# Optimization experiments

Hardware: AMD Instinct MI355X
Metric: run time of the kernel (lower is better)

## Reference

```python
import jax, jax.numpy as jnp
import numpy as np

C = 8            # number of categories (len(cat_id_radius_order_map_list))
S = 4            # segments per category
RADIUS_START = 1.0
RADIUS_DIFF = 1.0
MARGIN = -2.0    # cosine_emb_loss_margin; clamp(dot - MARGIN, 0) is identity since dot >= -1
RW = 0.5         # radius_loss_weight
SW = 0.5         # similarity_loss_weight
EPS = 1e-6


def setup_inputs() -> dict:
    key = jax.random.key(0)
    B, D, H, W = 4, 32, 512, 512
    outputs = jax.random.normal(key, (B, D, H, W), dtype=jnp.float32)
    # structured panoptic masks: C*S segments, contiguous in row-major flat order
    P = (H * W) // (C * S)                 # pixels per segment
    seg = (jnp.arange(H * W) // P).reshape(H, W).astype(jnp.int32)   # channel 0: segment id
    cat = (seg // S).astype(jnp.int32)                                # channel 1: category id
    inst = jnp.ones((H, W), jnp.int32)                                # channel 2: instance-discr flag (all True)
    masks = jnp.broadcast_to(jnp.stack([seg, cat, inst], axis=0)[None], (B, 3, H, W)).astype(jnp.int32)
    return {"outputs": outputs, "masks": masks, "annotations_data": 0}


def reference(outputs, masks, annotations_data):
    B, D, H, W = outputs.shape
    HW = H * W
    Sn = C * S
    P = HW // Sn
    emb = outputs.reshape(B, D, HW).transpose(0, 2, 1)          # [B, HW, D]
    seg_flat = masks[:, 0].reshape(B, HW)
    cat_flat = masks[:, 1].reshape(B, HW)
    radii = RADIUS_START + RADIUS_DIFF * jnp.arange(C, dtype=jnp.float32)

    # ---- radius loss: per-category MSE(||emb||_2, radius_cat), skipping the first unique cat (0)
    norms = jnp.linalg.norm(emb, axis=-1)                       # [B, HW]
    err = (norms - radii[cat_flat]) ** 2
    cat_all = cat_flat.reshape(-1)
    sums = jax.ops.segment_sum(err.reshape(-1), cat_all, num_segments=C)
    cnts = jax.ops.segment_sum(jnp.ones((B * HW,), jnp.float32), cat_all, num_segments=C)
    per_cat_mse = sums / cnts
    radius_loss = jnp.mean(per_cat_mse[1:])                     # unique_cat_ids[1:] -> cats 1..C-1

    # ---- gather pixels per segment; stable sort by segment id == boolean-mask gather order
    order = jnp.argsort(seg_flat, axis=1, stable=True)          # [B, HW]
    emb_sorted = jnp.take_along_axis(emb, order[..., None], axis=1)
    segs = emb_sorted.reshape(B, C, S, P, D)                    # segments grouped by category
    v = segs / (jnp.linalg.norm(segs, axis=-1, keepdims=True) + EPS)  # per-pixel L2-normalize

    count = P * (P + 1) / 2.0                                   # upper triangle incl diagonal

    # positives: mean over triu(incl diag) of (1 - v_i . v_j)
    #   sum_{triu} gram = (||sum_p v_p||^2 + sum_p ||v_p||^2) / 2
    T = jnp.sum(jnp.sum(v, axis=3) ** 2, axis=-1)               # [B, C, S]
    Dg = jnp.sum(v ** 2, axis=(3, 4))                           # [B, C, S]
    pos_mean = 1.0 - (T + Dg) / (2.0 * count)
    pos_total = jnp.sum(pos_mean)

    # negatives (same cat, segment pairs i<j): mean over triu(incl diag) of clamp(gram - MARGIN, 0)
    # clamp is inactive for MARGIN=-2; triu row-sum via reverse inclusive cumsum over pixels of j
    R = jnp.cumsum(v[:, :, :, ::-1, :], axis=3)[:, :, :, ::-1, :]     # [B, C, S, P, D]
    pair = jnp.einsum('bcipd,bcjpd->bcij', v, R)                # triu-sum of gram(curr=i, neg=j)
    iu, ju = jnp.triu_indices(S, k=1)
    neg_mean = pair[:, :, iu, ju] / count - MARGIN              # [B, C, S*(S-1)/2]
    neg_total = jnp.sum(neg_mean)

    sim_counter = B * C * (S + S * (S - 1) // 2)
    similarity_loss = (pos_total + neg_total) / sim_counter
    return RW * radius_loss + SW * similarity_loss
```

## Files before the change

### kernel.cpp

```cpp
#include <hip/hip_runtime.h>
#include <hip/hip_bf16.h>
#include <cstdint>

#define C_ 8
#define Bn 4
#define Dn 32
#define HWn 262144
#define Pn 8192
#define CH 256
#define NCH 32
#define NBLK (Bn*C_*NCH)
#define COUNTF 33558528.0f
#define CNT_PER_CAT 131072.0f

#define WS_SUM 0
#define WS_PART (NBLK*4*32)
#define WS_BC (WS_PART + NBLK*16)

__device__ __forceinline__ float wred(float x){
  #pragma unroll
  for (int off = 32; off; off >>= 1) x += __shfl_xor(x, off, 64);
  return x;
}

__device__ __forceinline__ unsigned int bfr(float x){
  __hip_bfloat16 h = __float2bfloat16(x);
  return (unsigned int)*reinterpret_cast<unsigned short*>(&h);
}

#define UNPK_LO(w) __uint_as_float((w) << 16)
#define UNPK_HI(w) __uint_as_float((w) & 0xffff0000u)

#define STEP(a0,a1,a2,a3) { \
  r0 += a0; r1 += a1; r2 += a2; r3 += a3; \
  p01 = fmaf(r0,a1,p01); p02 = fmaf(r0,a2,p02); p03 = fmaf(r0,a3,p03); \
  p12 = fmaf(r1,a2,p12); p13 = fmaf(r1,a3,p13); p23 = fmaf(r2,a3,p23); }

#define STEPW(w0,w1,w2,w3) { \
  STEP(UNPK_LO(w0), UNPK_LO(w1), UNPK_LO(w2), UNPK_LO(w3)); \
  STEP(UNPK_HI(w0), UNPK_HI(w1), UNPK_HI(w2), UNPK_HI(w3)); }

__global__ __launch_bounds__(256) void kA(const float* __restrict__ src, float* __restrict__ ws){
  __shared__ __align__(16) __hip_bfloat16 vbuf[4][32][264];
  __shared__ float lsum[4][32][8];
  __shared__ float redbuf[4][8];
  const int tid = threadIdx.x;
  const int blk = blockIdx.x;
  const int b = blk >> 8;
  const int c = (blk >> 5) & 7;
  const int k = blk & 31;
  const int j = tid >> 6;
  const int l = tid & 63;
  const float radius = 1.0f + (float)c;

  float errAcc = 0.0f, dgAcc = 0.0f;
  {
    const float* gp = src + (size_t)b*Dn*HWn + (size_t)(c*4+j)*Pn + (size_t)k*CH + l*4;
    float4 x[32];
    #pragma unroll
    for (int d = 0; d < 32; ++d) x[d] = *reinterpret_cast<const float4*>(gp + (size_t)d*HWn);
    float n0=0.f, n1=0.f, n2=0.f, n3=0.f;
    #pragma unroll
    for (int d = 0; d < 32; ++d){
      n0 = fmaf(x[d].x, x[d].x, n0); n1 = fmaf(x[d].y, x[d].y, n1);
      n2 = fmaf(x[d].z, x[d].z, n2); n3 = fmaf(x[d].w, x[d].w, n3);
    }
    float m0 = sqrtf(n0), m1 = sqrtf(n1), m2 = sqrtf(n2), m3 = sqrtf(n3);
    float i0 = 1.0f/(m0+1e-6f), i1 = 1.0f/(m1+1e-6f);
    float i2 = 1.0f/(m2+1e-6f), i3 = 1.0f/(m3+1e-6f);
    float e0 = m0-radius, e1 = m1-radius, e2 = m2-radius, e3 = m3-radius;
    errAcc = fmaf(e0,e0, fmaf(e1,e1, fmaf(e2,e2, e3*e3)));
    dgAcc  = fmaf(n0*i0,i0, fmaf(n1*i1,i1, fmaf(n2*i2,i2, (n3*i3)*i3)));
    #pragma unroll
    for (int d = 0; d < 32; ++d){
      unsigned int u0 = bfr(x[d].x*i0) | (bfr(x[d].y*i1) << 16);
      unsigned int u1 = bfr(x[d].z*i2) | (bfr(x[d].w*i3) << 16);
      *reinterpret_cast<uint2*>(&vbuf[j][d][l*4]) = make_uint2(u0, u1);
    }
  }
  __syncthreads();

  const int d = tid & 31;
  const int s = tid >> 5;
  float r0=0,r1=0,r2=0,r3=0;
  float p01=0,p02=0,p03=0,p12=0,p13=0,p23=0;
  {
    const uint4* s0p = (const uint4*)&vbuf[0][d][32*s];
    const uint4* s1p = (const uint4*)&vbuf[1][d][32*s];
    const uint4* s2p = (const uint4*)&vbuf[2][d][32*s];
    const uint4* s3p = (const uint4*)&vbuf[3][d][32*s];
    #pragma unroll
    for (int g = 0; g < 4; ++g){
      uint4 A = s0p[g], B = s1p[g], Cq = s2p[g], Dq = s3p[g];
      STEPW(A.x, B.x, Cq.x, Dq.x);
      STEPW(A.y, B.y, Cq.y, Dq.y);
      STEPW(A.z, B.z, Cq.z, Dq.z);
      STEPW(A.w, B.w, Cq.w, Dq.w);
    }
  }
  lsum[0][d][s] = r0; lsum[1][d][s] = r1; lsum[2][d][s] = r2; lsum[3][d][s] = r3;

  p01 = wred(p01); p02 = wred(p02); p03 = wred(p03);
  p12 = wred(p12); p13 = wred(p13); p23 = wred(p23);
  float dg = wred(dgAcc);
  float er = wred(errAcc);
  if ((tid & 63) == 0){
    const int w = tid >> 6;
    redbuf[w][0]=p01; redbuf[w][1]=p02; redbuf[w][2]=p03;
    redbuf[w][3]=p12; redbuf[w][4]=p13; redbuf[w][5]=p23;
    redbuf[w][6]=dg;  redbuf[w][7]=er;
  }
  __syncthreads();
  if (tid >= 64) return;

  float c0=0,c1=0,c2=0,c3=0;
  float x01=0,x02=0,x03=0,x12=0,x13=0,x23=0;
  {
    const int dd = tid & 31;
    #pragma unroll
    for (int ss = 0; ss < 8; ++ss){
      float a0=lsum[0][dd][ss], a1=lsum[1][dd][ss], a2=lsum[2][dd][ss], a3=lsum[3][dd][ss];
      x01=fmaf(c0,a1,x01); x02=fmaf(c0,a2,x02); x03=fmaf(c0,a3,x03);
      x12=fmaf(c1,a2,x12); x13=fmaf(c1,a3,x13); x23=fmaf(c2,a3,x23);
      c0+=a0; c1+=a1; c2+=a2; c3+=a3;
    }
    if (tid < 32){
      float* sp = ws + WS_SUM + (size_t)blk*128 + dd;
      sp[0]=c0; sp[32]=c1; sp[64]=c2; sp[96]=c3;
    }
  }
  x01 = 0.5f*wred(x01); x02 = 0.5f*wred(x02); x03 = 0.5f*wred(x03);
  x12 = 0.5f*wred(x12); x13 = 0.5f*wred(x13); x23 = 0.5f*wred(x23);
  if (tid == 0){
    float* pp = ws + WS_PART + (size_t)blk*16;
    pp[0] = redbuf[0][0]+redbuf[1][0]+redbuf[2][0]+redbuf[3][0] + x01;
    pp[1] = redbuf[0][1]+redbuf[1][1]+redbuf[2][1]+redbuf[3][1] + x02;
    pp[2] = redbuf[0][2]+redbuf[1][2]+redbuf[2][2]+redbuf[3][2] + x03;
    pp[3] = redbuf[0][3]+redbuf[1][3]+redbuf[2][3]+redbuf[3][3] + x12;
    pp[4] = redbuf[0][4]+redbuf[1][4]+redbuf[2][4]+redbuf[3][4] + x13;
    pp[5] = redbuf[0][5]+redbuf[1][5]+redbuf[2][5]+redbuf[3][5] + x23;
    pp[6] = redbuf[0][6]; pp[7] = redbuf[1][6];
    pp[8] = redbuf[2][6]; pp[9] = redbuf[3][6];
    pp[10] = redbuf[0][7]+redbuf[1][7]+redbuf[2][7]+redbuf[3][7];
  }
}

__global__ __launch_bounds__(64) void kB(float* __restrict__ ws){
  const int bc = blockIdx.x;
  const int lane = threadIdx.x;
  const int d = lane & 31;
  float c0=0,c1=0,c2=0,c3=0;
  float x01=0,x02=0,x03=0,x12=0,x13=0,x23=0;
  #pragma unroll 4
  for (int k = 0; k < 32; ++k){
    const float* sp = ws + WS_SUM + (size_t)(bc*32+k)*128 + d;
    float a0=sp[0], a1=sp[32], a2=sp[64], a3=sp[96];
    x01=fmaf(c0,a1,x01); x02=fmaf(c0,a2,x02); x03=fmaf(c0,a3,x03);
    x12=fmaf(c1,a2,x12); x13=fmaf(c1,a3,x13); x23=fmaf(c2,a3,x23);
    c0+=a0; c1+=a1; c2+=a2; c3+=a3;
  }
  float T0 = 0.5f*wred(c0*c0), T1 = 0.5f*wred(c1*c1);
  float T2 = 0.5f*wred(c2*c2), T3 = 0.5f*wred(c3*c3);
  x01=0.5f*wred(x01); x02=0.5f*wred(x02); x03=0.5f*wred(x03);
  x12=0.5f*wred(x12); x13=0.5f*wred(x13); x23=0.5f*wred(x23);

  const float* pp = ws + WS_PART + (size_t)(bc*32 + d)*16;
  float q0 = 0.5f*wred(pp[0]), q1 = 0.5f*wred(pp[1]), q2 = 0.5f*wred(pp[2]);
  float q3 = 0.5f*wred(pp[3]), q4 = 0.5f*wred(pp[4]), q5 = 0.5f*wred(pp[5]);
  float q6 = 0.5f*wred(pp[6]), q7 = 0.5f*wred(pp[7]), q8 = 0.5f*wred(pp[8]);
  float q9 = 0.5f*wred(pp[9]), q10 = 0.5f*wred(pp[10]);

  if (lane == 0){
    const float inv2c = 1.0f/(2.0f*COUNTF);
    const float invc  = 1.0f/COUNTF;
    float pos = (1.0f-(T0+q6)*inv2c) + (1.0f-(T1+q7)*inv2c)
              + (1.0f-(T2+q8)*inv2c) + (1.0f-(T3+q9)*inv2c);
    float neg = ((x01+q0)*invc + 2.0f) + ((x02+q1)*invc + 2.0f) + ((x03+q2)*invc + 2.0f)
              + ((x12+q3)*invc + 2.0f) + ((x13+q4)*invc + 2.0f) + ((x23+q5)*invc + 2.0f);
    float* o = ws + WS_BC + bc*3;
    o[0]=q10; o[1]=pos; o[2]=neg;
  }
}

__global__ __launch_bounds__(64) void kC(const float* __restrict__ ws, float* __restrict__ out){
  const int lane = threadIdx.x;
  float er = 0.f, pn = 0.f;
  if (lane < 32){
    const float* o = ws + WS_BC + lane*3;
    er = o[0]; pn = o[1] + o[2];
  }
  float sv = pn;
  #pragma unroll
  for (int off = 32; off; off >>= 1) sv += __shfl_xor(sv, off, 64);
  er += __shfl_xor(er, 8, 64);
  er += __shfl_xor(er, 16, 64);
  float r = (lane >= 1 && lane < 8) ? (er / CNT_PER_CAT) : 0.0f;
  r += __shfl_xor(r, 1, 64);
  r += __shfl_xor(r, 2, 64);
  r += __shfl_xor(r, 4, 64);
  if (lane == 0){
    float radius_loss = r / 7.0f;
    float sim = sv / 320.0f;
    out[0] = 0.5f*radius_loss + 0.5f*sim;
  }
}

extern "C" void kernel_launch(void* const* d_in, const int* in_sizes, int n_in,
                              void* d_out, int out_size, void* d_ws, size_t ws_size,
                              hipStream_t stream){
  const float* outputs = (const float*)d_in[0];
  float* ws  = (float*)d_ws;
  float* out = (float*)d_out;
  kA<<<NBLK, 256, 0, stream>>>(outputs, ws);
  kB<<<32, 64, 0, stream>>>(ws);
  kC<<<1, 64, 0, stream>>>(ws, out);
}
```

Before: 199.4 us.

## Split fused kernel into normalize-to-bf16 global stage and pair-product stage

```diff
diff --git a/kernel.cpp b/kernel.cpp
--- a/kernel.cpp
+++ b/kernel.cpp
@@ -1,5 +1,4 @@
 #include <hip/hip_runtime.h>
-#include <hip/hip_bf16.h>
 #include <cstdint>
 
 #define C_ 8
@@ -7,25 +6,19 @@
 #define Dn 32
 #define HWn 262144
 #define Pn 8192
-#define CH 256
-#define NCH 32
-#define NBLK (Bn*C_*NCH)
 #define COUNTF 33558528.0f
 #define CNT_PER_CAT 131072.0f
 
-#define WS_SUM 0
-#define WS_PART (NBLK*4*32)
-#define WS_BC (WS_PART + NBLK*16)
+#define WS_SUM  16777216
+#define WS_PART (WS_SUM + 131072)
+#define WS_DG   (WS_PART + 8192)
+#define WS_ERR  (WS_DG + 4096)
+#define WS_BC   (WS_ERR + 4096)
 
 __device__ __forceinline__ float wred(float x){
   #pragma unroll
   for (int off = 32; off; off >>= 1) x += __shfl_xor(x, off, 64);
   return x;
-}
-
-__device__ __forceinline__ unsigned int bfr(float x){
-  __hip_bfloat16 h = __float2bfloat16(x);
-  return (unsigned int)*reinterpret_cast<unsigned short*>(&h);
 }
 
 #define UNPK_LO(w) __uint_as_float((w) << 16)
@@ -40,55 +33,70 @@
   STEP(UNPK_LO(w0), UNPK_LO(w1), UNPK_LO(w2), UNPK_LO(w3)); \
   STEP(UNPK_HI(w0), UNPK_HI(w1), UNPK_HI(w2), UNPK_HI(w3)); }
 
-__global__ __launch_bounds__(256) void kA(const float* __restrict__ src, float* __restrict__ ws){
-  __shared__ __align__(16) __hip_bfloat16 vbuf[4][32][264];
-  __shared__ float lsum[4][32][8];
-  __shared__ float redbuf[4][8];
+__global__ __launch_bounds__(256) void kS(const float* __restrict__ src, float* __restrict__ ws){
   const int tid = threadIdx.x;
   const int blk = blockIdx.x;
-  const int b = blk >> 8;
-  const int c = (blk >> 5) & 7;
-  const int k = blk & 31;
-  const int j = tid >> 6;
-  const int l = tid & 63;
+  const int r = blk & 7;
+  const int j = (blk >> 3) & 3;
+  const int bc = blk >> 5;
+  const int b = bc >> 3, c = bc & 7;
+  const int w = tid >> 6;
+  const int k = (r << 2) | w;
+  const int pos = (r << 10) + tid * 4;
   const float radius = 1.0f + (float)c;
 
-  float errAcc = 0.0f, dgAcc = 0.0f;
-  {
-    const float* gp = src + (size_t)b*Dn*HWn + (size_t)(c*4+j)*Pn + (size_t)k*CH + l*4;
-    float4 x[32];
-    #pragma unroll
-    for (int d = 0; d < 32; ++d) x[d] = *reinterpret_cast<const float4*>(gp + (size_t)d*HWn);
-    float n0=0.f, n1=0.f, n2=0.f, n3=0.f;
-    #pragma unroll
-    for (int d = 0; d < 32; ++d){
-      n0 = fmaf(x[d].x, x[d].x, n0); n1 = fmaf(x[d].y, x[d].y, n1);
-      n2 = fmaf(x[d].z, x[d].z, n2); n3 = fmaf(x[d].w, x[d].w, n3);
-    }
-    float m0 = sqrtf(n0), m1 = sqrtf(n1), m2 = sqrtf(n2), m3 = sqrtf(n3);
-    float i0 = 1.0f/(m0+1e-6f), i1 = 1.0f/(m1+1e-6f);
-    float i2 = 1.0f/(m2+1e-6f), i3 = 1.0f/(m3+1e-6f);
-    float e0 = m0-radius, e1 = m1-radius, e2 = m2-radius, e3 = m3-radius;
-    errAcc = fmaf(e0,e0, fmaf(e1,e1, fmaf(e2,e2, e3*e3)));
-    dgAcc  = fmaf(n0*i0,i0, fmaf(n1*i1,i1, fmaf(n2*i2,i2, (n3*i3)*i3)));
-    #pragma unroll
-    for (int d = 0; d < 32; ++d){
-      unsigned int u0 = bfr(x[d].x*i0) | (bfr(x[d].y*i1) << 16);
-      unsigned int u1 = bfr(x[d].z*i2) | (bfr(x[d].w*i3) << 16);
-      *reinterpret_cast<uint2*>(&vbuf[j][d][l*4]) = make_uint2(u0, u1);
-    }
-  }
-  __syncthreads();
-
+  const float* base = src + (size_t)b*Dn*HWn + (size_t)(c*4+j)*Pn + pos;
+  float4 x[32];
+  #pragma unroll
+  for (int d = 0; d < 32; ++d) x[d] = *reinterpret_cast<const float4*>(base + (size_t)d*HWn);
+
+  float n0=0.f, n1=0.f, n2=0.f, n3=0.f;
+  #pragma unroll
+  for (int d = 0; d < 32; ++d){
+    n0 = fmaf(x[d].x, x[d].x, n0); n1 = fmaf(x[d].y, x[d].y, n1);
+    n2 = fmaf(x[d].z, x[d].z, n2); n3 = fmaf(x[d].w, x[d].w, n3);
+  }
+  float m0 = sqrtf(n0), m1 = sqrtf(n1), m2 = sqrtf(n2), m3 = sqrtf(n3);
+  float i0 = 1.0f/(m0+1e-6f), i1 = 1.0f/(m1+1e-6f);
+  float i2 = 1.0f/(m2+1e-6f), i3 = 1.0f/(m3+1e-6f);
+  float e0 = m0-radius, e1 = m1-radius, e2 = m2-radius, e3 = m3-radius;
+  float errAcc = fmaf(e0,e0, fmaf(e1,e1, fmaf(e2,e2, e3*e3)));
+  float dgAcc  = fmaf(n0*i0,i0, fmaf(n1*i1,i1, fmaf(n2*i2,i2, (n3*i3)*i3)));
+
+  unsigned short* vbase = (unsigned short*)ws;
+  const size_t eoff = ((((size_t)bc*32 + k)*4 + j)*32)*256 + (pos & 255);
+  #pragma unroll
+  for (int d = 0; d < 32; ++d){
+    uint2 u;
+    u.x = (__float_as_uint(x[d].x*i0) >> 16) | (__float_as_uint(x[d].y*i1) & 0xffff0000u);
+    u.y = (__float_as_uint(x[d].z*i2) >> 16) | (__float_as_uint(x[d].w*i3) & 0xffff0000u);
+    *reinterpret_cast<uint2*>(vbase + eoff + (size_t)d*256) = u;
+  }
+
+  float er = wred(errAcc);
+  float dg = wred(dgAcc);
+  if ((tid & 63) == 0){
+    ws[WS_DG  + bc*128 + j*32 + k] = dg;
+    ws[WS_ERR + bc*128 + j*32 + k] = er;
+  }
+}
+
+__global__ __launch_bounds__(256) void kP(float* __restrict__ ws){
+  __shared__ float lsum[4][32][8];
+  __shared__ float redbuf[4][6];
+  const int tid = threadIdx.x;
+  const int blk = blockIdx.x;
   const int d = tid & 31;
   const int s = tid >> 5;
+
+  const unsigned short* vb = (const unsigned short*)ws;
   float r0=0,r1=0,r2=0,r3=0;
   float p01=0,p02=0,p03=0,p12=0,p13=0,p23=0;
   {
-    const uint4* s0p = (const uint4*)&vbuf[0][d][32*s];
-    const uint4* s1p = (const uint4*)&vbuf[1][d][32*s];
-    const uint4* s2p = (const uint4*)&vbuf[2][d][32*s];
-    const uint4* s3p = (const uint4*)&vbuf[3][d][32*s];
+    const uint4* s0p = (const uint4*)(vb + (((size_t)blk*4 + 0)*32 + d)*256 + 32*s);
+    const uint4* s1p = (const uint4*)(vb + (((size_t)blk*4 + 1)*32 + d)*256 + 32*s);
+    const uint4* s2p = (const uint4*)(vb + (((size_t)blk*4 + 2)*32 + d)*256 + 32*s);
+    const uint4* s3p = (const uint4*)(vb + (((size_t)blk*4 + 3)*32 + d)*256 + 32*s);
     #pragma unroll
     for (int g = 0; g < 4; ++g){
       uint4 A = s0p[g], B = s1p[g], Cq = s2p[g], Dq = s3p[g];
@@ -102,13 +110,10 @@
 
   p01 = wred(p01); p02 = wred(p02); p03 = wred(p03);
   p12 = wred(p12); p13 = wred(p13); p23 = wred(p23);
-  float dg = wred(dgAcc);
-  float er = wred(errAcc);
   if ((tid & 63) == 0){
     const int w = tid >> 6;
     redbuf[w][0]=p01; redbuf[w][1]=p02; redbuf[w][2]=p03;
     redbuf[w][3]=p12; redbuf[w][4]=p13; redbuf[w][5]=p23;
-    redbuf[w][6]=dg;  redbuf[w][7]=er;
   }
   __syncthreads();
   if (tid >= 64) return;
@@ -132,16 +137,13 @@
   x01 = 0.5f*wred(x01); x02 = 0.5f*wred(x02); x03 = 0.5f*wred(x03);
   x12 = 0.5f*wred(x12); x13 = 0.5f*wred(x13); x23 = 0.5f*wred(x23);
   if (tid == 0){
-    float* pp = ws + WS_PART + (size_t)blk*16;
+    float* pp = ws + WS_PART + (size_t)blk*8;
     pp[0] = redbuf[0][0]+redbuf[1][0]+redbuf[2][0]+redbuf[3][0] + x01;
     pp[1] = redbuf[0][1]+redbuf[1][1]+redbuf[2][1]+redbuf[3][1] + x02;
     pp[2] = redbuf[0][2]+redbuf[1][2]+redbuf[2][2]+redbuf[3][2] + x03;
     pp[3] = redbuf[0][3]+redbuf[1][3]+redbuf[2][3]+redbuf[3][3] + x12;
     pp[4] = redbuf[0][4]+redbuf[1][4]+redbuf[2][4]+redbuf[3][4] + x13;
     pp[5] = redbuf[0][5]+redbuf[1][5]+redbuf[2][5]+redbuf[3][5] + x23;
-    pp[6] = redbuf[0][6]; pp[7] = redbuf[1][6];
-    pp[8] = redbuf[2][6]; pp[9] = redbuf[3][6];
-    pp[10] = redbuf[0][7]+redbuf[1][7]+redbuf[2][7]+redbuf[3][7];
   }
 }
 
@@ -164,21 +166,25 @@
   x01=0.5f*wred(x01); x02=0.5f*wred(x02); x03=0.5f*wred(x03);
   x12=0.5f*wred(x12); x13=0.5f*wred(x13); x23=0.5f*wred(x23);
 
-  const float* pp = ws + WS_PART + (size_t)(bc*32 + d)*16;
+  const float* pp = ws + WS_PART + (size_t)(bc*32 + d)*8;
   float q0 = 0.5f*wred(pp[0]), q1 = 0.5f*wred(pp[1]), q2 = 0.5f*wred(pp[2]);
   float q3 = 0.5f*wred(pp[3]), q4 = 0.5f*wred(pp[4]), q5 = 0.5f*wred(pp[5]);
-  float q6 = 0.5f*wred(pp[6]), q7 = 0.5f*wred(pp[7]), q8 = 0.5f*wred(pp[8]);
-  float q9 = 0.5f*wred(pp[9]), q10 = 0.5f*wred(pp[10]);
+
+  const float* dgp = ws + WS_DG  + bc*128;
+  const float* erp = ws + WS_ERR + bc*128;
+  float g0 = 0.5f*wred(dgp[d]),    g1 = 0.5f*wred(dgp[32+d]);
+  float g2 = 0.5f*wred(dgp[64+d]), g3 = 0.5f*wred(dgp[96+d]);
+  float er = 0.5f*wred(erp[d] + erp[32+d] + erp[64+d] + erp[96+d]);
 
   if (lane == 0){
     const float inv2c = 1.0f/(2.0f*COUNTF);
     const float invc  = 1.0f/COUNTF;
-    float pos = (1.0f-(T0+q6)*inv2c) + (1.0f-(T1+q7)*inv2c)
-              + (1.0f-(T2+q8)*inv2c) + (1.0f-(T3+q9)*inv2c);
+    float pos = (1.0f-(T0+g0)*inv2c) + (1.0f-(T1+g1)*inv2c)
+              + (1.0f-(T2+g2)*inv2c) + (1.0f-(T3+g3)*inv2c);
     float neg = ((x01+q0)*invc + 2.0f) + ((x02+q1)*invc + 2.0f) + ((x03+q2)*invc + 2.0f)
               + ((x12+q3)*invc + 2.0f) + ((x13+q4)*invc + 2.0f) + ((x23+q5)*invc + 2.0f);
     float* o = ws + WS_BC + bc*3;
-    o[0]=q10; o[1]=pos; o[2]=neg;
+    o[0]=er; o[1]=pos; o[2]=neg;
   }
 }
 
@@ -211,7 +217,8 @@
   const float* outputs = (const float*)d_in[0];
   float* ws  = (float*)d_ws;
   float* out = (float*)d_out;
-  kA<<<NBLK, 256, 0, stream>>>(outputs, ws);
+  kS<<<1024, 256, 0, stream>>>(outputs, ws);
+  kP<<<1024, 256, 0, stream>>>(ws);
   kB<<<32, 64, 0, stream>>>(ws);
   kC<<<1, 64, 0, stream>>>(ws, out);
 }
```

Result: slower. 231.8 us (+16.3%).

## Halve per-block chunk, use float2 loads and truncating bf16 pack

Applied to the files above, without the earlier changes.

```diff
diff --git a/kernel.cpp b/kernel.cpp
--- a/kernel.cpp
+++ b/kernel.cpp
@@ -1,5 +1,4 @@
 #include <hip/hip_runtime.h>
-#include <hip/hip_bf16.h>
 #include <cstdint>
 
 #define C_ 8
@@ -7,9 +6,10 @@
 #define Dn 32
 #define HWn 262144
 #define Pn 8192
-#define CH 256
-#define NCH 32
+#define CH 128
+#define NCH 64
 #define NBLK (Bn*C_*NCH)
+#define RL 136
 #define COUNTF 33558528.0f
 #define CNT_PER_CAT 131072.0f
 
@@ -23,11 +23,6 @@
   return x;
 }
 
-__device__ __forceinline__ unsigned int bfr(float x){
-  __hip_bfloat16 h = __float2bfloat16(x);
-  return (unsigned int)*reinterpret_cast<unsigned short*>(&h);
-}
-
 #define UNPK_LO(w) __uint_as_float((w) << 16)
 #define UNPK_HI(w) __uint_as_float((w) & 0xffff0000u)
 
@@ -40,42 +35,40 @@
   STEP(UNPK_LO(w0), UNPK_LO(w1), UNPK_LO(w2), UNPK_LO(w3)); \
   STEP(UNPK_HI(w0), UNPK_HI(w1), UNPK_HI(w2), UNPK_HI(w3)); }
 
-__global__ __launch_bounds__(256) void kA(const float* __restrict__ src, float* __restrict__ ws){
-  __shared__ __align__(16) __hip_bfloat16 vbuf[4][32][264];
+__global__ __launch_bounds__(256, 4) void kA(const float* __restrict__ src, float* __restrict__ ws){
+  __shared__ __align__(16) unsigned short vbuf[4][32][RL];
   __shared__ float lsum[4][32][8];
   __shared__ float redbuf[4][8];
   const int tid = threadIdx.x;
   const int blk = blockIdx.x;
-  const int b = blk >> 8;
-  const int c = (blk >> 5) & 7;
-  const int k = blk & 31;
+  const int bc = blk >> 6;
+  const int k = blk & 63;
+  const int b = bc >> 3;
+  const int c = bc & 7;
   const int j = tid >> 6;
   const int l = tid & 63;
   const float radius = 1.0f + (float)c;
 
-  float errAcc = 0.0f, dgAcc = 0.0f;
+  float errAcc, dgAcc;
   {
-    const float* gp = src + (size_t)b*Dn*HWn + (size_t)(c*4+j)*Pn + (size_t)k*CH + l*4;
-    float4 x[32];
-    #pragma unroll
-    for (int d = 0; d < 32; ++d) x[d] = *reinterpret_cast<const float4*>(gp + (size_t)d*HWn);
-    float n0=0.f, n1=0.f, n2=0.f, n3=0.f;
+    const float* gp = src + (size_t)b*Dn*HWn + (size_t)(c*4+j)*Pn + (k<<7) + (l<<1);
+    float2 x[32];
+    #pragma unroll
+    for (int d = 0; d < 32; ++d) x[d] = *reinterpret_cast<const float2*>(gp + (size_t)d*HWn);
+    float n0=0.f, n1=0.f;
     #pragma unroll
     for (int d = 0; d < 32; ++d){
       n0 = fmaf(x[d].x, x[d].x, n0); n1 = fmaf(x[d].y, x[d].y, n1);
-      n2 = fmaf(x[d].z, x[d].z, n2); n3 = fmaf(x[d].w, x[d].w, n3);
-    }
-    float m0 = sqrtf(n0), m1 = sqrtf(n1), m2 = sqrtf(n2), m3 = sqrtf(n3);
+    }
+    float m0 = sqrtf(n0), m1 = sqrtf(n1);
     float i0 = 1.0f/(m0+1e-6f), i1 = 1.0f/(m1+1e-6f);
-    float i2 = 1.0f/(m2+1e-6f), i3 = 1.0f/(m3+1e-6f);
-    float e0 = m0-radius, e1 = m1-radius, e2 = m2-radius, e3 = m3-radius;
-    errAcc = fmaf(e0,e0, fmaf(e1,e1, fmaf(e2,e2, e3*e3)));
-    dgAcc  = fmaf(n0*i0,i0, fmaf(n1*i1,i1, fmaf(n2*i2,i2, (n3*i3)*i3)));
+    float e0 = m0-radius, e1 = m1-radius;
+    errAcc = fmaf(e0,e0, e1*e1);
+    dgAcc  = fmaf(n0*i0,i0, (n1*i1)*i1);
     #pragma unroll
     for (int d = 0; d < 32; ++d){
-      unsigned int u0 = bfr(x[d].x*i0) | (bfr(x[d].y*i1) << 16);
-      unsigned int u1 = bfr(x[d].z*i2) | (bfr(x[d].w*i3) << 16);
-      *reinterpret_cast<uint2*>(&vbuf[j][d][l*4]) = make_uint2(u0, u1);
+      unsigned int u = (__float_as_uint(x[d].x*i0) >> 16) | (__float_as_uint(x[d].y*i1) & 0xffff0000u);
+      *reinterpret_cast<unsigned int*>(&vbuf[j][d][2*l]) = u;
     }
   }
   __syncthreads();
@@ -85,12 +78,12 @@
   float r0=0,r1=0,r2=0,r3=0;
   float p01=0,p02=0,p03=0,p12=0,p13=0,p23=0;
   {
-    const uint4* s0p = (const uint4*)&vbuf[0][d][32*s];
-    const uint4* s1p = (const uint4*)&vbuf[1][d][32*s];
-    const uint4* s2p = (const uint4*)&vbuf[2][d][32*s];
-    const uint4* s3p = (const uint4*)&vbuf[3][d][32*s];
-    #pragma unroll
-    for (int g = 0; g < 4; ++g){
+    const uint4* s0p = (const uint4*)&vbuf[0][d][16*s];
+    const uint4* s1p = (const uint4*)&vbuf[1][d][16*s];
+    const uint4* s2p = (const uint4*)&vbuf[2][d][16*s];
+    const uint4* s3p = (const uint4*)&vbuf[3][d][16*s];
+    #pragma unroll
+    for (int g = 0; g < 2; ++g){
       uint4 A = s0p[g], B = s1p[g], Cq = s2p[g], Dq = s3p[g];
       STEPW(A.x, B.x, Cq.x, Dq.x);
       STEPW(A.y, B.y, Cq.y, Dq.y);
@@ -152,8 +145,8 @@
   float c0=0,c1=0,c2=0,c3=0;
   float x01=0,x02=0,x03=0,x12=0,x13=0,x23=0;
   #pragma unroll 4
-  for (int k = 0; k < 32; ++k){
-    const float* sp = ws + WS_SUM + (size_t)(bc*32+k)*128 + d;
+  for (int k = 0; k < NCH; ++k){
+    const float* sp = ws + WS_SUM + (size_t)(bc*NCH+k)*128 + d;
     float a0=sp[0], a1=sp[32], a2=sp[64], a3=sp[96];
     x01=fmaf(c0,a1,x01); x02=fmaf(c0,a2,x02); x03=fmaf(c0,a3,x03);
     x12=fmaf(c1,a2,x12); x13=fmaf(c1,a3,x13); x23=fmaf(c2,a3,x23);
@@ -164,11 +157,11 @@
   x01=0.5f*wred(x01); x02=0.5f*wred(x02); x03=0.5f*wred(x03);
   x12=0.5f*wred(x12); x13=0.5f*wred(x13); x23=0.5f*wred(x23);
 
-  const float* pp = ws + WS_PART + (size_t)(bc*32 + d)*16;
-  float q0 = 0.5f*wred(pp[0]), q1 = 0.5f*wred(pp[1]), q2 = 0.5f*wred(pp[2]);
-  float q3 = 0.5f*wred(pp[3]), q4 = 0.5f*wred(pp[4]), q5 = 0.5f*wred(pp[5]);
-  float q6 = 0.5f*wred(pp[6]), q7 = 0.5f*wred(pp[7]), q8 = 0.5f*wred(pp[8]);
-  float q9 = 0.5f*wred(pp[9]), q10 = 0.5f*wred(pp[10]);
+  const float* pp = ws + WS_PART + (size_t)(bc*NCH + lane)*16;
+  float q0 = wred(pp[0]), q1 = wred(pp[1]), q2 = wred(pp[2]);
+  float q3 = wred(pp[3]), q4 = wred(pp[4]), q5 = wred(pp[5]);
+  float q6 = wred(pp[6]), q7 = wred(pp[7]), q8 = wred(pp[8]);
+  float q9 = wred(pp[9]), q10 = wred(pp[10]);
 
   if (lane == 0){
     const float inv2c = 1.0f/(2.0f*COUNTF);
```

After: 202.9 us. Within noise of the previous version (+1.8%).
